# Optimization experiments

Hardware: AMD Instinct MI355X
Metric: run time of the kernel (lower is better)

## Reference

```python
import jax, jax.numpy as jnp
import numpy as np

B, S, E, H = 4, 2048, 1024, 16
D = E // H  # head_dim = 64

def setup_inputs() -> dict:
    key = jax.random.key(0)
    ks = jax.random.split(key, 9)
    std = 1.0 / np.sqrt(E)
    return {
        "x":  jax.random.normal(ks[0], (B, S, E), jnp.float32),
        "Wq": jax.random.uniform(ks[1], (E, E), jnp.float32, -std, std),
        "bq": jax.random.uniform(ks[2], (E,),   jnp.float32, -std, std),
        "Wk": jax.random.uniform(ks[3], (E, E), jnp.float32, -std, std),
        "bk": jax.random.uniform(ks[4], (E,),   jnp.float32, -std, std),
        "Wv": jax.random.uniform(ks[5], (E, E), jnp.float32, -std, std),
        "bv": jax.random.uniform(ks[6], (E,),   jnp.float32, -std, std),
        "Wo": jax.random.uniform(ks[7], (E, E), jnp.float32, -std, std),
        "bo": jax.random.uniform(ks[8], (E,),   jnp.float32, -std, std),
    }

def reference(x, Wq, bq, Wk, bk, Wv, bv, Wo, bo):
    b, s, e = x.shape
    # QKV projections (weights stored as [in,out] == torch W.T applied as x @ W)
    q = (x @ Wq + bq).reshape(b, s, H, D).transpose(0, 2, 1, 3)  # [B,H,S,D]
    k = (x @ Wk + bk).reshape(b, s, H, D).transpose(0, 2, 1, 3)
    v = (x @ Wv + bv).reshape(b, s, H, D).transpose(0, 2, 1, 3)
    scores = jnp.einsum('bhqd,bhkd->bhqk', q, k) / jnp.sqrt(jnp.float32(D))
    causal = jnp.triu(jnp.ones((s, s), bool), k=1)  # True above diagonal
    scores = jnp.where(causal, -jnp.inf, scores)
    p = jax.nn.softmax(scores, axis=-1)  # dropout disabled (eval mode)
    out = jnp.einsum('bhqk,bhkd->bhqd', p, v)  # [B,H,S,D]
    out = out.transpose(0, 2, 1, 3).reshape(b, s, e)
    return out @ Wo + bo
```

## Files before the change

kernel.cpp:

```cpp
#include <hip/hip_runtime.h>
#include <math.h>

#define E_DIM 1024
#define B_DIM 4
#define S_DIM 2048
#define H_DIM 16
#define D_HEAD 64
#define M_DIM (B_DIM * S_DIM)
#define LOG2E 1.44269504f

typedef _Float16 half8 __attribute__((ext_vector_type(8)));
typedef _Float16 half4 __attribute__((ext_vector_type(4)));
typedef __fp16  fp16x2 __attribute__((ext_vector_type(2)));
typedef float floatx4 __attribute__((ext_vector_type(4)));
#define MFMA_F16(a, b, c) __builtin_amdgcn_mfma_f32_16x16x32_f16(a, b, c, 0, 0, 0)

#if __has_builtin(__builtin_amdgcn_exp2f)
#define EXP2F(x) __builtin_amdgcn_exp2f(x)
#else
#define EXP2F(x) exp2f(x)
#endif

union H4 { fp16x2 h2[2]; half4 h4; };

#define GLDS16(g, l)                                                          \
    __builtin_amdgcn_global_load_lds(                                         \
        (const __attribute__((address_space(1))) void*)(g),                   \
        (__attribute__((address_space(3))) void*)(l), 16, 0, 0)

__device__ const int SEG_QBLK[40] = {3,4,5,6,7,7,8,8,9,9,10,10,11,11,11,12,12,12,
                                     13,13,13,14,14,14,15,15,15,15,
                                     2,6,10,14, 1,5,9,13, 0,4,8,12};
__device__ const int SEG_SEG[40]  = {0,0,0,0,0,1,0,1,0,1,0,1,0,1,2,0,1,2,
                                     0,1,2,0,1,2,0,1,2,3,
                                     0,1,2,3, 0,1,2,3, 0,1,2,3};
__device__ const int SEG_BASE[16] = {0,1,2,3,4,6,8,10,12,15,18,21,24,28,32,36};

__global__ __launch_bounds__(256) void cvt_x(
    const float* __restrict__ X, _Float16* __restrict__ Xh)
{
    size_t i = ((size_t)blockIdx.x * 256 + threadIdx.x) * 8;
    float4 a = *(const float4*)&X[i];
    float4 b = *(const float4*)&X[i + 4];
    half8 h = {(_Float16)a.x, (_Float16)a.y, (_Float16)a.z, (_Float16)a.w,
               (_Float16)b.x, (_Float16)b.y, (_Float16)b.z, (_Float16)b.w};
    *(half8*)&Xh[i] = h;
}

__global__ __launch_bounds__(256) void cvt_w(
    const float* __restrict__ W0, const float* __restrict__ W1,
    const float* __restrict__ W2, const float* __restrict__ W3,
    _Float16* __restrict__ T0, _Float16* __restrict__ T1,
    _Float16* __restrict__ T2, _Float16* __restrict__ T3)
{
    const int z = blockIdx.z;
    const float* W = (z == 0) ? W0 : (z == 1) ? W1 : (z == 2) ? W2 : W3;
    _Float16*   T  = (z == 0) ? T0 : (z == 1) ? T1 : (z == 2) ? T2 : T3;
    const int k0 = blockIdx.x * 64, n0 = blockIdx.y * 64;
    const int tid = threadIdx.x;
    __shared__ float t[64][65];
#pragma unroll
    for (int it = 0; it < 4; it++) {
        int r = it * 16 + (tid >> 4);
        int c = (tid & 15) * 4;
        float4 v = *(const float4*)&W[(size_t)(k0 + r) * E_DIM + n0 + c];
        t[r][c] = v.x; t[r][c + 1] = v.y; t[r][c + 2] = v.z; t[r][c + 3] = v.w;
    }
    __syncthreads();
#pragma unroll
    for (int it = 0; it < 2; it++) {
        int n = it * 32 + (tid >> 3);
        int kk = (tid & 7) * 8;
        half8 h;
#pragma unroll
        for (int j = 0; j < 8; j++) h[j] = (_Float16)t[kk + j][n];
        *(half8*)&T[(size_t)(n0 + n) * E_DIM + k0 + kk] = h;
    }
}

#define GEMM_CORE(Aptr, Bptr)                                                 \
    const int tid = threadIdx.x;                                              \
    const int wave = tid >> 6, lane = tid & 63;                               \
    const int m16 = lane & 15, quad = lane >> 4;                              \
    const int wm = (wave >> 1) * 64, wn = (wave & 1) * 64;                    \
    const int m0 = blockIdx.x * 128, n0 = blockIdx.y * 128;                   \
    __shared__ _Float16 As[128 * 32];                                         \
    __shared__ _Float16 Bs[128 * 32];                                         \
    floatx4 acc[4][4];                                                        \
    const floatx4 zf = {0.f, 0.f, 0.f, 0.f};                                  \
    _Pragma("unroll") for (int i = 0; i < 4; i++)                             \
        _Pragma("unroll") for (int j = 0; j < 4; j++) acc[i][j] = zf;         \
    const int lrow = lane >> 2, lseg = lane & 3;                              \
    const _Float16* gA = (Aptr) + (size_t)(m0 + wave * 32 + lrow) * E_DIM + lseg * 8; \
    const _Float16* gB = (Bptr) + (size_t)(n0 + wave * 32 + lrow) * E_DIM + lseg * 8; \
    _Float16* lA = As + (wave * 32) * 32;                                     \
    _Float16* lB = Bs + (wave * 32) * 32;                                     \
    for (int k0 = 0; k0 < E_DIM; k0 += 32) {                                  \
        __syncthreads();                                                      \
        GLDS16(gA + k0, lA);                                                  \
        GLDS16(gA + 16 * E_DIM + k0, lA + 16 * 32);                           \
        GLDS16(gB + k0, lB);                                                  \
        GLDS16(gB + 16 * E_DIM + k0, lB + 16 * 32);                           \
        __syncthreads();                                                      \
        half8 af[4], bf[4];                                                   \
        _Pragma("unroll") for (int mt = 0; mt < 4; mt++)                      \
            af[mt] = *(const half8*)&As[(wm + mt * 16 + m16) * 32 + quad * 8];\
        _Pragma("unroll") for (int nt = 0; nt < 4; nt++)                      \
            bf[nt] = *(const half8*)&Bs[(wn + nt * 16 + m16) * 32 + quad * 8];\
        _Pragma("unroll") for (int mt = 0; mt < 4; mt++)                      \
            _Pragma("unroll") for (int nt = 0; nt < 4; nt++)                  \
                acc[mt][nt] = MFMA_F16(af[mt], bf[nt], acc[mt][nt]);          \
    }

__global__ __launch_bounds__(256) void qkv_mfma(
    const _Float16* __restrict__ Xh,
    const _Float16* __restrict__ Tq, const float* __restrict__ bq,
    const _Float16* __restrict__ Tk, const float* __restrict__ bk,
    const _Float16* __restrict__ Tv, const float* __restrict__ bv,
    _Float16* __restrict__ Qo, _Float16* __restrict__ Ko, _Float16* __restrict__ Vo)
{
    const int z = blockIdx.z;
    const _Float16* Wt   = (z == 0) ? Tq : (z == 1) ? Tk : Tv;
    const float*    bias = (z == 0) ? bq : (z == 1) ? bk : bv;

    GEMM_CORE(Xh, Wt)

    if (z == 2) {
#pragma unroll
        for (int nt = 0; nt < 4; nt++) {
            int n = n0 + wn + nt * 16 + m16;
            int h = n >> 6, d = n & 63, d7 = n & 7;
            float bias_v = bias[n];
#pragma unroll
            for (int mt = 0; mt < 4; mt++) {
                int m_b = m0 + wm + mt * 16 + quad * 4;
                int b = m_b >> 11, s = m_b & 2047;
                int bh = b * H_DIM + h;
                size_t off = ((size_t)bh * 32 + (s >> 6)) * 4096
                           + (size_t)d * 64 + ((((s >> 3) & 7) ^ d7) * 8) + (s & 7);
                half4 hv;
#pragma unroll
                for (int r = 0; r < 4; r++) hv[r] = (_Float16)(acc[mt][nt][r] + bias_v);
                *(half4*)&Vo[off] = hv;
            }
        }
    } else {
        _Float16* Out = (z == 0) ? Qo : Ko;
        const float sc = (z == 0) ? 0.125f * LOG2E : 1.0f;
#pragma unroll
        for (int nt = 0; nt < 4; nt++) {
            int n = n0 + wn + nt * 16 + m16;
            int h = n >> 6;
            int db = (n >> 3) & 7, d7 = n & 7;
            float bias_v = bias[n];
#pragma unroll
            for (int mt = 0; mt < 4; mt++) {
#pragma unroll
                for (int r = 0; r < 4; r++) {
                    int m = m0 + wm + mt * 16 + quad * 4 + r;
                    int b = m >> 11, s = m & 2047;
                    int bh = b * H_DIM + h;
                    size_t off;
                    if (z == 0)
                        off = ((size_t)bh * 16 + (s >> 7)) * 8192
                            + (size_t)(s & 127) * 64 + ((db ^ (s & 7)) * 8) + d7;
                    else
                        off = ((size_t)bh * 32 + (s >> 6)) * 4096
                            + (size_t)(s & 63) * 64 + ((db ^ (s & 7)) * 8) + d7;
                    Out[off] = (_Float16)((acc[mt][nt][r] + bias_v) * sc);
                }
            }
        }
    }
}

__global__ __launch_bounds__(256) void out_mfma(
    const _Float16* __restrict__ Oh, const _Float16* __restrict__ To,
    const float* __restrict__ bias, float* __restrict__ Out)
{
    GEMM_CORE(Oh, To)

#pragma unroll
    for (int nt = 0; nt < 4; nt++) {
        int n = n0 + wn + nt * 16 + m16;
        float bias_v = bias[n];
#pragma unroll
        for (int mt = 0; mt < 4; mt++) {
#pragma unroll
            for (int r = 0; r < 4; r++) {
                int m = m0 + wm + mt * 16 + quad * 4 + r;
                Out[(size_t)m * E_DIM + n] = acc[mt][nt][r] + bias_v;
            }
        }
    }
}

__global__ __launch_bounds__(256) void attn_mfma(
    const _Float16* __restrict__ Qb, const _Float16* __restrict__ Kb,
    const _Float16* __restrict__ Vb, _Float16* __restrict__ Opart,
    float* __restrict__ Mv, float* __restrict__ Lv, _Float16* __restrict__ O)
{
    const int bh = blockIdx.y;
    const int wid = blockIdx.x;
    const int qblk = SEG_QBLK[wid];
    const int seg  = SEG_SEG[wid];
    const int q0 = qblk * 128;
    const int c0 = seg * 8;
    const int c1 = min(c0 + 8, 2 * qblk + 2);
    const bool solo = (c0 == 0) && (c1 == 2 * qblk + 2);
    const int tid = threadIdx.x;
    const int wave = tid >> 6, lane = tid & 63;
    const int m16 = lane & 15, quad = lane >> 4;
    const int sw = m16 & 7;

    __shared__ _Float16 QP[8192];
    __shared__ _Float16 KsA[8192];
    __shared__ _Float16 VsA[8192];

    const _Float16* gQ = Qb + ((size_t)bh * 16 + qblk) * 8192;
#pragma unroll
    for (int t = 0; t < 4; t++) {
        int i = wave * 4 + t;
        GLDS16(gQ + i * 512 + lane * 8, QP + i * 512);
    }

    const _Float16* kp = Kb + (size_t)bh * 131072 + (size_t)c0 * 4096 + wave * 1024 + lane * 8;
    const _Float16* vp = Vb + (size_t)bh * 131072 + (size_t)c0 * 4096 + wave * 1024 + lane * 8;
    _Float16* dK = KsA + wave * 1024;
    _Float16* dV = VsA + wave * 1024;
    {
        int b0 = (c0 & 1) * 4096;
        GLDS16(kp, dK + b0);  GLDS16(kp + 512, dK + b0 + 512);
        GLDS16(vp, dV + b0);  GLDS16(vp + 512, dV + b0 + 512);
    }
    __syncthreads();

    half8 qf[2][2];
#pragma unroll
    for (int mt = 0; mt < 2; mt++)
#pragma unroll
        for (int dh = 0; dh < 2; dh++)
            qf[mt][dh] = *(const half8*)&QP[(wave * 32 + mt * 16 + m16) * 64
                                            + (((dh * 4 + quad) ^ sw) * 8)];

    int ko[4][2], vo[4][2];
#pragma unroll
    for (int kt = 0; kt < 4; kt++) {
        ko[kt][0] = (kt * 16 + m16) * 64 + ((quad ^ sw) << 3);
        ko[kt][1] = (kt * 16 + m16) * 64 + (((quad + 4) ^ sw) << 3);
        vo[kt][0] = ko[kt][0];
        vo[kt][1] = ko[kt][1];
    }
    _Float16* Pw = QP + wave * 2048;
    _Float16* pwp[2][4];
    const _Float16* pfp[2][2];
#pragma unroll
    for (int mt = 0; mt < 2; mt++) {
#pragma unroll
        for (int kt = 0; kt < 4; kt++) {
            int kb = kt * 2 + (quad >> 1);
            pwp[mt][kt] = &Pw[(mt * 16 + m16) * 64 + ((kb ^ sw) << 3) + ((quad & 1) << 2)];
        }
#pragma unroll
        for (int kh = 0; kh < 2; kh++)
            pfp[mt][kh] = &Pw[(mt * 16 + m16) * 64 + (((kh * 4 + quad) ^ sw) << 3)];
    }

    float m_i[2] = {-INFINITY, -INFINITY}, l_i[2] = {0.f, 0.f};
    floatx4 acco[2][4];
    const floatx4 zf = {0.f, 0.f, 0.f, 0.f};
#pragma unroll
    for (int mt = 0; mt < 2; mt++)
#pragma unroll
        for (int dt = 0; dt < 4; dt++) acco[mt][dt] = zf;

    const int qmin = q0 + wave * 32;
    const int qmax = qmin + 31;

    for (int c = c0; c < c1; c++) {
        const int boff = (c & 1) * 4096;
        if (c + 1 < c1) {
            kp += 4096; vp += 4096;
            int b1 = boff ^ 4096;
            GLDS16(kp, dK + b1);  GLDS16(kp + 512, dK + b1 + 512);
            GLDS16(vp, dV + b1);  GLDS16(vp + 512, dV + b1 + 512);
        }
        const int k0 = c * 64;
        if (k0 <= qmax) {
            floatx4 sf[2][4];
#pragma unroll
            for (int kt = 0; kt < 4; kt++) {
                half8 kf0 = *(const half8*)&KsA[boff + ko[kt][0]];
                half8 kf1 = *(const half8*)&KsA[boff + ko[kt][1]];
#pragma unroll
                for (int mt = 0; mt < 2; mt++)
                    sf[mt][kt] = MFMA_F16(kf1, qf[mt][1], MFMA_F16(kf0, qf[mt][0], zf));
            }

            const bool full = (k0 + 63 <= qmin);
#pragma unroll
            for (int mt = 0; mt < 2; mt++) {
                const int qg = qmin + mt * 16 + m16;
                float p[4][4];
                float mx = -INFINITY;
#pragma unroll
                for (int kt = 0; kt < 4; kt++)
#pragma unroll
                    for (int r = 0; r < 4; r++) {
                        float v = sf[mt][kt][r];
                        if (!full) {
                            int key = k0 + kt * 16 + quad * 4 + r;
                            v = (key <= qg) ? v : -INFINITY;
                        }
                        p[kt][r] = v;
                        mx = fmaxf(mx, v);
                    }
                mx = fmaxf(mx, __shfl_xor(mx, 16));
                mx = fmaxf(mx, __shfl_xor(mx, 32));
                float mn = fmaxf(m_i[mt], mx);
                float alpha = EXP2F(m_i[mt] - mn);
                m_i[mt] = mn;
                float ls = 0.f;
#pragma unroll
                for (int kt = 0; kt < 4; kt++)
#pragma unroll
                    for (int r = 0; r < 4; r++) {
                        float e = EXP2F(p[kt][r] - mn);
                        p[kt][r] = e;
                        ls += e;
                    }
                ls += __shfl_xor(ls, 16);
                ls += __shfl_xor(ls, 32);
                l_i[mt] = l_i[mt] * alpha + ls;
#pragma unroll
                for (int dt = 0; dt < 4; dt++) acco[mt][dt] *= alpha;

#pragma unroll
                for (int kt = 0; kt < 4; kt++) {
                    H4 u;
                    u.h2[0] = __builtin_amdgcn_cvt_pkrtz(p[kt][0], p[kt][1]);
                    u.h2[1] = __builtin_amdgcn_cvt_pkrtz(p[kt][2], p[kt][3]);
                    *(half4*)pwp[mt][kt] = u.h4;
                }
            }
            asm volatile("s_waitcnt lgkmcnt(0)" ::: "memory");

            half8 pf[2][2];
#pragma unroll
            for (int mt = 0; mt < 2; mt++)
#pragma unroll
                for (int kh = 0; kh < 2; kh++)
                    pf[mt][kh] = *(const half8*)pfp[mt][kh];
#pragma unroll
            for (int dt = 0; dt < 4; dt++) {
                half8 vf0 = *(const half8*)&VsA[boff + vo[dt][0]];
                half8 vf1 = *(const half8*)&VsA[boff + vo[dt][1]];
#pragma unroll
                for (int mt = 0; mt < 2; mt++)
                    acco[mt][dt] = MFMA_F16(vf1, pf[mt][1],
                                    MFMA_F16(vf0, pf[mt][0], acco[mt][dt]));
            }
        }
        __syncthreads();
    }

    if (solo) {
        const int b = bh >> 4;
        const int h = bh & (H_DIM - 1);
#pragma unroll
        for (int mt = 0; mt < 2; mt++) {
            float inv = 1.f / l_i[mt];
            int q = qmin + mt * 16 + m16;
            _Float16* dst = O + (size_t)(b * S_DIM + q) * E_DIM + h * 64;
#pragma unroll
            for (int dt = 0; dt < 4; dt++) {
                H4 u;
                u.h2[0] = __builtin_amdgcn_cvt_pkrtz(acco[mt][dt][0] * inv, acco[mt][dt][1] * inv);
                u.h2[1] = __builtin_amdgcn_cvt_pkrtz(acco[mt][dt][2] * inv, acco[mt][dt][3] * inv);
                *(half4*)&dst[dt * 16 + quad * 4] = u.h4;
            }
        }
    } else {
        const size_t prow = ((size_t)bh * 40 + SEG_BASE[qblk] + seg) * 128;
#pragma unroll
        for (int mt = 0; mt < 2; mt++) {
            int lq = wave * 32 + mt * 16 + m16;
            if (quad == 0) {
                Mv[prow + lq] = m_i[mt];
                Lv[prow + lq] = l_i[mt];
            }
            _Float16* dst = Opart + (prow + lq) * 64;
#pragma unroll
            for (int dt = 0; dt < 4; dt++) {
                H4 u;
                u.h2[0] = __builtin_amdgcn_cvt_pkrtz(acco[mt][dt][0], acco[mt][dt][1]);
                u.h2[1] = __builtin_amdgcn_cvt_pkrtz(acco[mt][dt][2], acco[mt][dt][3]);
                *(half4*)&dst[dt * 16 + quad * 4] = u.h4;
            }
        }
    }
}

__global__ __launch_bounds__(256) void attn_combine(
    const _Float16* __restrict__ Opart, const float* __restrict__ Mv,
    const float* __restrict__ Lv, _Float16* __restrict__ O)
{
    const int qb = blockIdx.x + 4, bh = blockIdx.y;
    const int nseg = (qb >> 2) + 1;
    const size_t pbase = ((size_t)bh * 40 + SEG_BASE[qb]) * 128;
    const int t = threadIdx.x;
    const int r = t >> 1, dh = (t & 1) * 32;

    float m_s[4], w[4];
    float M = -INFINITY;
    for (int s = 0; s < nseg; s++) {
        m_s[s] = Mv[pbase + s * 128 + r];
        M = fmaxf(M, m_s[s]);
    }
    float L = 0.f;
    for (int s = 0; s < nseg; s++) {
        w[s] = EXP2F(m_s[s] - M);
        L += Lv[pbase + s * 128 + r] * w[s];
    }
    const float invL = 1.f / L;

    const int b = bh >> 4, h = bh & (H_DIM - 1);
    const int q = qb * 128 + r;
    _Float16* dst = O + (size_t)(b * S_DIM + q) * E_DIM + h * 64 + dh;
#pragma unroll
    for (int d0 = 0; d0 < 32; d0 += 8) {
        float acc[8] = {0.f, 0.f, 0.f, 0.f, 0.f, 0.f, 0.f, 0.f};
        for (int s = 0; s < nseg; s++) {
            half8 v = *(const half8*)&Opart[(pbase + s * 128 + r) * 64 + dh + d0];
#pragma unroll
            for (int j = 0; j < 8; j++) acc[j] += w[s] * (float)v[j];
        }
        half8 o;
#pragma unroll
        for (int j = 0; j < 8; j++) o[j] = (_Float16)(acc[j] * invL);
        *(half8*)&dst[d0] = o;
    }
}

extern "C" void kernel_launch(void* const* d_in, const int* in_sizes, int n_in,
                              void* d_out, int out_size, void* d_ws, size_t ws_size,
                              hipStream_t stream) {
    const float* x  = (const float*)d_in[0];
    const float* Wq = (const float*)d_in[1];
    const float* bq = (const float*)d_in[2];
    const float* Wk = (const float*)d_in[3];
    const float* bk = (const float*)d_in[4];
    const float* Wv = (const float*)d_in[5];
    const float* bv = (const float*)d_in[6];
    const float* Wo = (const float*)d_in[7];
    const float* bo = (const float*)d_in[8];

    const size_t SZ = (size_t)M_DIM * E_DIM;
    const size_t WZ = (size_t)E_DIM * E_DIM;
    _Float16* Xh = (_Float16*)d_ws;
    _Float16* Tq = Xh + SZ;
    _Float16* Tk = Tq + WZ;
    _Float16* Tv = Tk + WZ;
    _Float16* To = Tv + WZ;
    _Float16* Qb = To + WZ;
    _Float16* Kb = Qb + SZ;
    _Float16* Vb = Kb + SZ;
    _Float16* Opart = Vb + SZ;
    float* Mv = (float*)(Opart + (size_t)2560 * 8192);
    float* Lv = Mv + 2560 * 128;
    _Float16* Oh = Xh;

    cvt_x<<<dim3(M_DIM * E_DIM / 2048), 256, 0, stream>>>(x, Xh);
    cvt_w<<<dim3(16, 16, 4), 256, 0, stream>>>(Wq, Wk, Wv, Wo, Tq, Tk, Tv, To);

    qkv_mfma<<<dim3(M_DIM / 128, E_DIM / 128, 3), 256, 0, stream>>>(
        Xh, Tq, bq, Tk, bk, Tv, bv, Qb, Kb, Vb);

    attn_mfma<<<dim3(40, B_DIM * H_DIM), 256, 0, stream>>>(
        Qb, Kb, Vb, Opart, Mv, Lv, Oh);

    attn_combine<<<dim3(12, B_DIM * H_DIM), 256, 0, stream>>>(Opart, Mv, Lv, Oh);

    out_mfma<<<dim3(M_DIM / 128, E_DIM / 128), 256, 0, stream>>>(
        Oh, To, bo, (float*)d_out);
}
```

Baseline: 297.9 us.

## Load attention Q/K/V fragments directly from global in MFMA-ready layout

The QKV projection epilogue now writes Q, K and V in a pre-fragmented layout that matches the MFMA operand order, so the attention kernel can load fragments straight from global memory into registers. This drops the shared-memory staging of K/V, the per-tile __syncthreads, and the double buffering, and trims each wave's loop to the chunks its own query rows need. It also adds a lazy softmax rescale that skips the alpha correction when the running max grows by less than a threshold, plus s_setprio around the MFMA blocks. In exchange, each wave re-reads K/V from global/L2 with no sharing across the block's waves, and the loads are prefetched through registers only.

```diff
diff --git a/kernel.cpp b/kernel.cpp
--- a/kernel.cpp
+++ b/kernel.cpp
@@ -8,6 +8,7 @@
 #define D_HEAD 64
 #define M_DIM (B_DIM * S_DIM)
 #define LOG2E 1.44269504f
+#define RESCALE_THR 4.0f
 
 typedef _Float16 half8 __attribute__((ext_vector_type(8)));
 typedef _Float16 half4 __attribute__((ext_vector_type(4)));
@@ -129,15 +130,18 @@
 #pragma unroll
         for (int nt = 0; nt < 4; nt++) {
             int n = n0 + wn + nt * 16 + m16;
-            int h = n >> 6, d = n & 63, d7 = n & 7;
+            int h = n >> 6, d = n & 63;
+            int dt = d >> 4, ld = d & 15;
             float bias_v = bias[n];
 #pragma unroll
             for (int mt = 0; mt < 4; mt++) {
                 int m_b = m0 + wm + mt * 16 + quad * 4;
                 int b = m_b >> 11, s = m_b & 2047;
                 int bh = b * H_DIM + h;
-                size_t off = ((size_t)bh * 32 + (s >> 6)) * 4096
-                           + (size_t)d * 64 + ((((s >> 3) & 7) ^ d7) * 8) + (s & 7);
+                int c = s >> 6, kl = s & 63;
+                int kh = kl >> 5, q8 = (kl >> 3) & 3, j0 = kl & 7;
+                size_t off = ((size_t)bh * 32 + c) * 4096
+                           + (size_t)(((dt * 2 + kh) * 64 + q8 * 16 + ld) * 8 + j0);
                 half4 hv;
 #pragma unroll
                 for (int r = 0; r < 4; r++) hv[r] = (_Float16)(acc[mt][nt][r] + bias_v);
@@ -150,8 +154,8 @@
 #pragma unroll
         for (int nt = 0; nt < 4; nt++) {
             int n = n0 + wn + nt * 16 + m16;
-            int h = n >> 6;
-            int db = (n >> 3) & 7, d7 = n & 7;
+            int h = n >> 6, d = n & 63;
+            int dh = d >> 5, qd = (d >> 3) & 3, j = d & 7;
             float bias_v = bias[n];
 #pragma unroll
             for (int mt = 0; mt < 4; mt++) {
@@ -161,12 +165,17 @@
                     int b = m >> 11, s = m & 2047;
                     int bh = b * H_DIM + h;
                     size_t off;
-                    if (z == 0)
-                        off = ((size_t)bh * 16 + (s >> 7)) * 8192
-                            + (size_t)(s & 127) * 64 + ((db ^ (s & 7)) * 8) + d7;
-                    else
-                        off = ((size_t)bh * 32 + (s >> 6)) * 4096
-                            + (size_t)(s & 63) * 64 + ((db ^ (s & 7)) * 8) + d7;
+                    if (z == 0) {
+                        int qblk = s >> 7, qq = s & 127;
+                        int sub = qq >> 4, lq = qq & 15;
+                        off = ((size_t)bh * 16 + qblk) * 8192
+                            + (size_t)(((sub * 2 + dh) * 64 + qd * 16 + lq) * 8 + j);
+                    } else {
+                        int c = s >> 6, kl = s & 63;
+                        int kt = kl >> 4, lk = kl & 15;
+                        off = ((size_t)bh * 32 + c) * 4096
+                            + (size_t)(((kt * 2 + dh) * 64 + qd * 16 + lk) * 8 + j);
+                    }
                     Out[off] = (_Float16)((acc[mt][nt][r] + bias_v) * sc);
                 }
             }
@@ -213,45 +222,21 @@
     const int m16 = lane & 15, quad = lane >> 4;
     const int sw = m16 & 7;
 
-    __shared__ _Float16 QP[8192];
-    __shared__ _Float16 KsA[8192];
-    __shared__ _Float16 VsA[8192];
-
-    const _Float16* gQ = Qb + ((size_t)bh * 16 + qblk) * 8192;
-#pragma unroll
-    for (int t = 0; t < 4; t++) {
-        int i = wave * 4 + t;
-        GLDS16(gQ + i * 512 + lane * 8, QP + i * 512);
-    }
-
-    const _Float16* kp = Kb + (size_t)bh * 131072 + (size_t)c0 * 4096 + wave * 1024 + lane * 8;
-    const _Float16* vp = Vb + (size_t)bh * 131072 + (size_t)c0 * 4096 + wave * 1024 + lane * 8;
-    _Float16* dK = KsA + wave * 1024;
-    _Float16* dV = VsA + wave * 1024;
-    {
-        int b0 = (c0 & 1) * 4096;
-        GLDS16(kp, dK + b0);  GLDS16(kp + 512, dK + b0 + 512);
-        GLDS16(vp, dV + b0);  GLDS16(vp + 512, dV + b0 + 512);
-    }
-    __syncthreads();
-
+    __shared__ _Float16 Ps[8192];
+    _Float16* Pw = Ps + wave * 2048;
+
+    const int qmin = q0 + wave * 32;
+    const int qmax = qmin + 31;
+    const int c1w = min(c1, (qmax >> 6) + 1);
+
+    const _Float16* gQ = Qb + ((size_t)bh * 16 + qblk) * 8192 + wave * 2048 + lane * 8;
     half8 qf[2][2];
 #pragma unroll
     for (int mt = 0; mt < 2; mt++)
 #pragma unroll
         for (int dh = 0; dh < 2; dh++)
-            qf[mt][dh] = *(const half8*)&QP[(wave * 32 + mt * 16 + m16) * 64
-                                            + (((dh * 4 + quad) ^ sw) * 8)];
-
-    int ko[4][2], vo[4][2];
-#pragma unroll
-    for (int kt = 0; kt < 4; kt++) {
-        ko[kt][0] = (kt * 16 + m16) * 64 + ((quad ^ sw) << 3);
-        ko[kt][1] = (kt * 16 + m16) * 64 + (((quad + 4) ^ sw) << 3);
-        vo[kt][0] = ko[kt][0];
-        vo[kt][1] = ko[kt][1];
-    }
-    _Float16* Pw = QP + wave * 2048;
+            qf[mt][dh] = *(const half8*)&gQ[(mt * 2 + dh) * 512];
+
     _Float16* pwp[2][4];
     const _Float16* pfp[2][2];
 #pragma unroll
@@ -274,94 +259,108 @@
 #pragma unroll
         for (int dt = 0; dt < 4; dt++) acco[mt][dt] = zf;
 
-    const int qmin = q0 + wave * 32;
-    const int qmax = qmin + 31;
-
-    for (int c = c0; c < c1; c++) {
-        const int boff = (c & 1) * 4096;
-        if (c + 1 < c1) {
-            kp += 4096; vp += 4096;
-            int b1 = boff ^ 4096;
-            GLDS16(kp, dK + b1);  GLDS16(kp + 512, dK + b1 + 512);
-            GLDS16(vp, dV + b1);  GLDS16(vp + 512, dV + b1 + 512);
-        }
+    const _Float16* gK = Kb + ((size_t)bh * 32 + c0) * 4096 + lane * 8;
+    const _Float16* gV = Vb + ((size_t)bh * 32 + c0) * 4096 + lane * 8;
+
+    half8 kf[4][2];
+#pragma unroll
+    for (int kt = 0; kt < 4; kt++)
+#pragma unroll
+        for (int dh = 0; dh < 2; dh++)
+            kf[kt][dh] = *(const half8*)&gK[(kt * 2 + dh) * 512];
+    gK += 4096;
+
+    for (int c = c0; c < c1w; c++) {
         const int k0 = c * 64;
-        if (k0 <= qmax) {
-            floatx4 sf[2][4];
-#pragma unroll
-            for (int kt = 0; kt < 4; kt++) {
-                half8 kf0 = *(const half8*)&KsA[boff + ko[kt][0]];
-                half8 kf1 = *(const half8*)&KsA[boff + ko[kt][1]];
-#pragma unroll
-                for (int mt = 0; mt < 2; mt++)
-                    sf[mt][kt] = MFMA_F16(kf1, qf[mt][1], MFMA_F16(kf0, qf[mt][0], zf));
-            }
-
-            const bool full = (k0 + 63 <= qmin);
-#pragma unroll
-            for (int mt = 0; mt < 2; mt++) {
-                const int qg = qmin + mt * 16 + m16;
-                float p[4][4];
-                float mx = -INFINITY;
-#pragma unroll
-                for (int kt = 0; kt < 4; kt++)
-#pragma unroll
-                    for (int r = 0; r < 4; r++) {
-                        float v = sf[mt][kt][r];
-                        if (!full) {
-                            int key = k0 + kt * 16 + quad * 4 + r;
-                            v = (key <= qg) ? v : -INFINITY;
-                        }
-                        p[kt][r] = v;
-                        mx = fmaxf(mx, v);
+
+        half8 vf[4][2];
+#pragma unroll
+        for (int dt = 0; dt < 4; dt++)
+#pragma unroll
+            for (int kh = 0; kh < 2; kh++)
+                vf[dt][kh] = *(const half8*)&gV[(dt * 2 + kh) * 512];
+        gV += 4096;
+
+        floatx4 sf[2][4];
+        __builtin_amdgcn_s_setprio(1);
+#pragma unroll
+        for (int kt = 0; kt < 4; kt++)
+#pragma unroll
+            for (int mt = 0; mt < 2; mt++)
+                sf[mt][kt] = MFMA_F16(kf[kt][1], qf[mt][1],
+                               MFMA_F16(kf[kt][0], qf[mt][0], zf));
+        __builtin_amdgcn_s_setprio(0);
+
+        if (c + 1 < c1w) {
+#pragma unroll
+            for (int kt = 0; kt < 4; kt++)
+#pragma unroll
+                for (int dh = 0; dh < 2; dh++)
+                    kf[kt][dh] = *(const half8*)&gK[(kt * 2 + dh) * 512];
+            gK += 4096;
+        }
+
+        const bool full = (k0 + 63 <= qmin);
+#pragma unroll
+        for (int mt = 0; mt < 2; mt++) {
+            const int qg = qmin + mt * 16 + m16;
+            float mx = -INFINITY;
+#pragma unroll
+            for (int kt = 0; kt < 4; kt++)
+#pragma unroll
+                for (int r = 0; r < 4; r++) {
+                    float v = sf[mt][kt][r];
+                    if (!full) {
+                        int key = k0 + kt * 16 + quad * 4 + r;
+                        v = (key <= qg) ? v : -INFINITY;
                     }
-                mx = fmaxf(mx, __shfl_xor(mx, 16));
-                mx = fmaxf(mx, __shfl_xor(mx, 32));
-                float mn = fmaxf(m_i[mt], mx);
+                    sf[mt][kt][r] = v;
+                    mx = fmaxf(mx, v);
+                }
+            mx = fmaxf(mx, __shfl_xor(mx, 16));
+            mx = fmaxf(mx, __shfl_xor(mx, 32));
+            float mn = m_i[mt];
+            if (!__all(mx <= mn + RESCALE_THR)) {
+                mn = fmaxf(mn, mx);
                 float alpha = EXP2F(m_i[mt] - mn);
                 m_i[mt] = mn;
-                float ls = 0.f;
-#pragma unroll
-                for (int kt = 0; kt < 4; kt++)
-#pragma unroll
-                    for (int r = 0; r < 4; r++) {
-                        float e = EXP2F(p[kt][r] - mn);
-                        p[kt][r] = e;
-                        ls += e;
-                    }
-                ls += __shfl_xor(ls, 16);
-                ls += __shfl_xor(ls, 32);
-                l_i[mt] = l_i[mt] * alpha + ls;
+                l_i[mt] *= alpha;
 #pragma unroll
                 for (int dt = 0; dt < 4; dt++) acco[mt][dt] *= alpha;
-
-#pragma unroll
-                for (int kt = 0; kt < 4; kt++) {
-                    H4 u;
-                    u.h2[0] = __builtin_amdgcn_cvt_pkrtz(p[kt][0], p[kt][1]);
-                    u.h2[1] = __builtin_amdgcn_cvt_pkrtz(p[kt][2], p[kt][3]);
-                    *(half4*)pwp[mt][kt] = u.h4;
-                }
-            }
-            asm volatile("s_waitcnt lgkmcnt(0)" ::: "memory");
-
-            half8 pf[2][2];
+            }
+            float ls = 0.f;
+#pragma unroll
+            for (int kt = 0; kt < 4; kt++) {
+                float e0 = EXP2F(sf[mt][kt][0] - mn);
+                float e1 = EXP2F(sf[mt][kt][1] - mn);
+                float e2 = EXP2F(sf[mt][kt][2] - mn);
+                float e3 = EXP2F(sf[mt][kt][3] - mn);
+                ls += (e0 + e1) + (e2 + e3);
+                H4 u;
+                u.h2[0] = __builtin_amdgcn_cvt_pkrtz(e0, e1);
+                u.h2[1] = __builtin_amdgcn_cvt_pkrtz(e2, e3);
+                *(half4*)pwp[mt][kt] = u.h4;
+            }
+            ls += __shfl_xor(ls, 16);
+            ls += __shfl_xor(ls, 32);
+            l_i[mt] += ls;
+        }
+        asm volatile("s_waitcnt lgkmcnt(0)" ::: "memory");
+
+        half8 pf[2][2];
+#pragma unroll
+        for (int mt = 0; mt < 2; mt++)
+#pragma unroll
+            for (int kh = 0; kh < 2; kh++)
+                pf[mt][kh] = *(const half8*)pfp[mt][kh];
+        __builtin_amdgcn_s_setprio(1);
+#pragma unroll
+        for (int dt = 0; dt < 4; dt++)
 #pragma unroll
             for (int mt = 0; mt < 2; mt++)
-#pragma unroll
-                for (int kh = 0; kh < 2; kh++)
-                    pf[mt][kh] = *(const half8*)pfp[mt][kh];
-#pragma unroll
-            for (int dt = 0; dt < 4; dt++) {
-                half8 vf0 = *(const half8*)&VsA[boff + vo[dt][0]];
-                half8 vf1 = *(const half8*)&VsA[boff + vo[dt][1]];
-#pragma unroll
-                for (int mt = 0; mt < 2; mt++)
-                    acco[mt][dt] = MFMA_F16(vf1, pf[mt][1],
-                                    MFMA_F16(vf0, pf[mt][0], acco[mt][dt]));
-            }
-        }
-        __syncthreads();
+                acco[mt][dt] = MFMA_F16(vf[dt][1], pf[mt][1],
+                                 MFMA_F16(vf[dt][0], pf[mt][0], acco[mt][dt]));
+        __builtin_amdgcn_s_setprio(0);
     }
 
     if (solo) {
```

After: 305.8 us. 2.6% more time.
